# Performance work log

Hardware: AMD Instinct MI355X
Metric: run time of the kernel (lower is better)

The kernel has to match this reference:

```python
import jax, jax.numpy as jnp
import numpy as np

B, N, M = 2, 8192, 8192


def setup_inputs() -> dict:
    key = jax.random.key(0)
    ks = jax.random.split(key, 6)
    return {
        "predicted_points": jax.random.normal(ks[0], (B, N, 3), dtype=jnp.float32),
        "predicted_sdfs": jax.random.normal(ks[1], (B, N, 1), dtype=jnp.float32),
        "predicted_colors": jax.random.uniform(ks[2], (B, N, 3), dtype=jnp.float32),
        "ref_points": jax.random.normal(ks[3], (B, M, 3), dtype=jnp.float32),
        "ref_sdfs": jax.random.normal(ks[4], (B, M, 1), dtype=jnp.float32),
        "ref_colors": jax.random.uniform(ks[5], (B, M, 3), dtype=jnp.float32),
    }


def reference(predicted_points, predicted_sdfs, predicted_colors,
              ref_points, ref_sdfs, ref_colors):
    # Squared pairwise distances [B, N, M]; monotonic in cdist, so argmin/min
    # match torch.cdist-based results (chamfer_distance uses squared dists).
    d2 = (jnp.sum(predicted_points ** 2, axis=-1)[:, :, None]
          + jnp.sum(ref_points ** 2, axis=-1)[:, None, :]
          - 2.0 * jnp.einsum("bnd,bmd->bnm", predicted_points, ref_points))
    d2 = jnp.maximum(d2, 0.0)

    # Faithful to original: argmin over dim=1 -> nearest PREDICTED point index
    # for each ref point, shape [B, M]; then gathers into ref_sdfs/ref_colors.
    closest = jnp.argmin(d2, axis=1)  # [B, M], values in [0, N)

    gathered_sdfs = jnp.take_along_axis(ref_sdfs, closest[..., None], axis=1)  # [B, M, 1]
    sdf_l1 = jnp.mean(jnp.abs(gathered_sdfs - predicted_sdfs))

    gathered_colors = jnp.take_along_axis(ref_colors, closest[..., None], axis=1)  # [B, M, 3]
    color_l1 = jnp.mean(jnp.abs(gathered_colors - predicted_colors))

    # pytorch3d chamfer_distance: mean over points of squared min dists in both
    # directions, summed, then mean over batch.
    cham_xy = jnp.mean(jnp.min(d2, axis=2), axis=1)  # pred -> ref, [B]
    cham_yx = jnp.mean(jnp.min(d2, axis=1), axis=1)  # ref -> pred, [B]
    chamfer = jnp.mean(cham_xy + cham_yx)

    # [sdf_l1_loss, color_l1_loss, chamfer_distance_loss]
    return jnp.stack([sdf_l1, color_l1, chamfer])
```

## Files before the change

kernel.cpp:

```cpp
#include <hip/hip_runtime.h>
#include <cstdint>
#include <cstddef>

#define B_ 2
#define N_ 8192
#define M_ 8192
#define COLSPLIT 8
#define CCHUNK (N_ / COLSPLIT)
#define NTILES (CCHUNK / 32)
#define ROWBLKS (M_ / 128)
#define RBLOCKS ((B_ * M_) / 256)

typedef __attribute__((ext_vector_type(8))) short short8;
typedef __attribute__((ext_vector_type(16))) float f32x16;

union FragU { uint4 u; short8 s; };

__device__ __forceinline__ unsigned bf16r(float f) {
    unsigned u = __float_as_uint(f);
    return ((u + 0x7FFFu + ((u >> 16) & 1u)) >> 16) & 0xFFFFu;
}
#define BF_ONE 0x3F80u

__device__ __forceinline__ unsigned umin_(unsigned a, unsigned b) { return a < b ? a : b; }
__device__ __forceinline__ unsigned long long ullmin_(unsigned long long a, unsigned long long b) { return a < b ? a : b; }

__global__ __launch_bounds__(256) void k_init(uint4* __restrict__ p)
{
    const int i = blockIdx.x * 256 + threadIdx.x;
    uint4 v = {0xFFFFFFFFu, 0xFFFFFFFFu, 0xFFFFFFFFu, 0xFFFFFFFFu};
    p[i] = v;
}

__global__ __launch_bounds__(256, 4) void k_pairs(
    const float* __restrict__ pred_pts,
    const float* __restrict__ ref_pts,
    unsigned long long* __restrict__ rowpart,
    unsigned int* __restrict__ colminU,
    float* __restrict__ out)
{
    __shared__ uint4 ldsB[CCHUNK + 1];
    __shared__ unsigned int ldsCol[CCHUNK];

    const int t    = threadIdx.x;
    const int wave = t >> 6;
    const int lane = t & 63;
    const int l31  = lane & 31;
    const int half = lane >> 5;
    const int rowblk  = blockIdx.x;
    const int cs      = blockIdx.y;
    const int colbase = cs * CCHUNK;
    const int b       = blockIdx.z;

    if (rowblk == 0 && cs == 0 && b == 0 && t == 0) {
        out[0] = 0.f; out[1] = 0.f; out[2] = 0.f;
    }

    for (int i = t; i < CCHUNK; i += 256) {
        const float* p = pred_pts + ((size_t)b * N_ + colbase + i) * 3;
        float x = p[0], y = p[1], z = p[2];
        float nrm = x * x + y * y + z * z;
        unsigned nh = bf16r(nrm);
        unsigned nl = bf16r(nrm - __uint_as_float(nh << 16));
        uint4 v;
        v.x = bf16r(-2.f * x) | (bf16r(-2.f * y) << 16);
        v.y = bf16r(-2.f * z) | (BF_ONE << 16);
        v.z = BF_ONE | (nh << 16);
        v.w = nl;
        ldsB[i] = v;
        ldsCol[i] = 0xFFFFFFFFu;
    }
    if (t == 0) { uint4 z4 = {0, 0, 0, 0}; ldsB[CCHUNK] = z4; }

    FragU af; af.u.x = af.u.y = af.u.z = af.u.w = 0;
    const int rowbase = rowblk * 128 + wave * 32;
    if (half == 0) {
        const float* r = ref_pts + ((size_t)b * M_ + rowbase + l31) * 3;
        float x = r[0], y = r[1], z = r[2];
        float nrm = x * x + y * y + z * z;
        unsigned nh = bf16r(nrm);
        unsigned nl = bf16r(nrm - __uint_as_float(nh << 16));
        af.u.x = bf16r(x) | (bf16r(y) << 16);
        af.u.y = bf16r(z) | (nh << 16);
        af.u.z = nl | (BF_ONE << 16);
        af.u.w = BF_ONE;
    }
    __syncthreads();

    f32x16 zero16 = {};
    unsigned rowbest[16];
    #pragma unroll
    for (int i = 0; i < 16; ++i) rowbest[i] = 0xFFFFFFFFu;

    const int bslot = (half == 0) ? l31 : CCHUNK;
    const int bstep = (half == 0) ? 32 : 0;

    #pragma unroll 2
    for (int tile = 0; tile < NTILES; tile += 2) {
        FragU b0; b0.u = ldsB[bslot + tile * bstep];
        FragU b1; b1.u = ldsB[bslot + (tile + 1) * bstep];
        f32x16 acc0 = __builtin_amdgcn_mfma_f32_32x32x16_bf16(af.s, b0.s, zero16, 0, 0, 0);
        f32x16 acc1 = __builtin_amdgcn_mfma_f32_32x32x16_bf16(af.s, b1.s, zero16, 0, 0, 0);

        const unsigned lcol0 = (unsigned)(tile * 32 + l31);
        const unsigned lcol1 = lcol0 + 32;
        #pragma unroll
        for (int i = 0; i < 16; ++i) {
            unsigned pk0 = (__float_as_uint(acc0[i]) & 0xFFFFF800u) | lcol0;
            unsigned pk1 = (__float_as_uint(acc1[i]) & 0xFFFFF800u) | lcol1;
            rowbest[i] = umin_(rowbest[i], umin_(pk0, pk1));
        }
        float c0 = fminf(fminf(fminf(fminf(acc0[0], acc0[1]), fminf(acc0[2], acc0[3])),
                               fminf(fminf(acc0[4], acc0[5]), fminf(acc0[6], acc0[7]))),
                         fminf(fminf(fminf(acc0[8], acc0[9]), fminf(acc0[10], acc0[11])),
                               fminf(fminf(acc0[12], acc0[13]), fminf(acc0[14], acc0[15]))));
        float c1 = fminf(fminf(fminf(fminf(acc1[0], acc1[1]), fminf(acc1[2], acc1[3])),
                               fminf(fminf(acc1[4], acc1[5]), fminf(acc1[6], acc1[7]))),
                         fminf(fminf(fminf(acc1[8], acc1[9]), fminf(acc1[10], acc1[11])),
                               fminf(fminf(acc1[12], acc1[13]), fminf(acc1[14], acc1[15]))));
        atomicMin(&ldsCol[lcol0], __float_as_uint(c0));
        atomicMin(&ldsCol[lcol1], __float_as_uint(c1));
    }

    unsigned long long* rdst = rowpart + (size_t)(b * COLSPLIT + cs) * M_;
    #pragma unroll
    for (int i = 0; i < 16; ++i) {
        unsigned pk = rowbest[i];
        #pragma unroll
        for (int off = 1; off < 32; off <<= 1) {
            unsigned o = __shfl_xor(pk, off);
            pk = o < pk ? o : pk;
        }
        if (l31 == 0) {
            int row = rowbase + (i & 3) + 8 * (i >> 2) + 4 * half;
            rdst[row] = ((unsigned long long)(pk & 0xFFFFF800u) << 32)
                        | (unsigned)(colbase + (pk & 0x7FFu));
        }
    }

    __syncthreads();
    for (int i = t; i < CCHUNK; i += 256)
        atomicMin(&colminU[(size_t)b * N_ + colbase + i], ldsCol[i]);
}

__global__ __launch_bounds__(256) void k_reduce(
    const unsigned long long* __restrict__ rowpart,
    const unsigned int* __restrict__ colminU,
    const float* __restrict__ pred_sdfs,
    const float* __restrict__ pred_cols,
    const float* __restrict__ ref_sdfs,
    const float* __restrict__ ref_cols,
    float* __restrict__ out)
{
    __shared__ float wsum[4][3];
    const int i = blockIdx.x * 256 + threadIdx.x;
    const int b = i >> 13;
    const int m = i & (M_ - 1);

    unsigned long long pk = 0xFFFFFFFFFFFFFFFFull;
    #pragma unroll
    for (int s = 0; s < COLSPLIT; ++s)
        pk = ullmin_(pk, rowpart[(size_t)(b * COLSPLIT + s) * M_ + m]);

    unsigned cm = colminU[i];

    float chyx = fmaxf(__uint_as_float((unsigned)(pk >> 32)), 0.f);
    int arg = (int)(unsigned)(pk & 0xFFFFFFFFull);
    float chxy = fmaxf(__uint_as_float(cm), 0.f);

    float sdf = fabsf(ref_sdfs[(size_t)b * M_ + arg] - pred_sdfs[i]);
    const float* rc = ref_cols + ((size_t)b * M_ + arg) * 3;
    const float* pc = pred_cols + (size_t)i * 3;
    float col = fabsf(rc[0] - pc[0]) + fabsf(rc[1] - pc[1]) + fabsf(rc[2] - pc[2]);

    float cham = chyx * (1.f / (B_ * M_)) + chxy * (1.f / (B_ * N_));
    sdf *= 1.f / (B_ * M_);
    col *= 1.f / (B_ * M_ * 3);

    #pragma unroll
    for (int off = 32; off > 0; off >>= 1) {
        sdf  += __shfl_down(sdf, off);
        col  += __shfl_down(col, off);
        cham += __shfl_down(cham, off);
    }
    const int wave = threadIdx.x >> 6;
    if ((threadIdx.x & 63) == 0) {
        wsum[wave][0] = sdf; wsum[wave][1] = col; wsum[wave][2] = cham;
    }
    __syncthreads();
    if (threadIdx.x == 0) {
        atomicAdd(&out[0], wsum[0][0] + wsum[1][0] + wsum[2][0] + wsum[3][0]);
        atomicAdd(&out[1], wsum[0][1] + wsum[1][1] + wsum[2][1] + wsum[3][1]);
        atomicAdd(&out[2], wsum[0][2] + wsum[1][2] + wsum[2][2] + wsum[3][2]);
    }
}

extern "C" void kernel_launch(void* const* d_in, const int* in_sizes, int n_in,
                              void* d_out, int out_size, void* d_ws, size_t ws_size,
                              hipStream_t stream) {
    const float* pred_pts  = (const float*)d_in[0];
    const float* pred_sdfs = (const float*)d_in[1];
    const float* pred_cols = (const float*)d_in[2];
    const float* ref_pts   = (const float*)d_in[3];
    const float* ref_sdfs  = (const float*)d_in[4];
    const float* ref_cols  = (const float*)d_in[5];
    float* out = (float*)d_out;

    char* ws = (char*)d_ws;
    unsigned long long* rowpart = (unsigned long long*)ws;
    unsigned int* colminU = (unsigned int*)(ws + (size_t)B_ * COLSPLIT * M_ * 8);

    k_init<<<16, 256, 0, stream>>>((uint4*)colminU);

    dim3 g1(ROWBLKS, COLSPLIT, B_);
    k_pairs<<<g1, 256, 0, stream>>>(pred_pts, ref_pts, rowpart, colminU, out);

    k_reduce<<<RBLOCKS, 256, 0, stream>>>(
        rowpart, colminU, pred_sdfs, pred_cols, ref_sdfs, ref_cols, out);
}
```

Baseline: 90.61 us.

## Precompute bf16 point fragments once and double the column split

```diff
diff --git a/kernel.cpp b/kernel.cpp
--- a/kernel.cpp
+++ b/kernel.cpp
@@ -5,7 +5,7 @@
 #define B_ 2
 #define N_ 8192
 #define M_ 8192
-#define COLSPLIT 8
+#define COLSPLIT 16
 #define CCHUNK (N_ / COLSPLIT)
 #define NTILES (CCHUNK / 32)
 #define ROWBLKS (M_ / 128)
@@ -25,19 +25,55 @@
 __device__ __forceinline__ unsigned umin_(unsigned a, unsigned b) { return a < b ? a : b; }
 __device__ __forceinline__ unsigned long long ullmin_(unsigned long long a, unsigned long long b) { return a < b ? a : b; }
 
-__global__ __launch_bounds__(256) void k_init(uint4* __restrict__ p)
+__global__ __launch_bounds__(256) void k_init(
+    const float* __restrict__ pred_pts,
+    const float* __restrict__ ref_pts,
+    uint4* __restrict__ predB,
+    uint4* __restrict__ refA,
+    uint4* __restrict__ colminU4,
+    float* __restrict__ out)
 {
     const int i = blockIdx.x * 256 + threadIdx.x;
-    uint4 v = {0xFFFFFFFFu, 0xFFFFFFFFu, 0xFFFFFFFFu, 0xFFFFFFFFu};
-    p[i] = v;
+
+    if (i == 0) { out[0] = 0.f; out[1] = 0.f; out[2] = 0.f; }
+    if (i < (B_ * N_) / 4) {
+        uint4 v = {0xFFFFFFFFu, 0xFFFFFFFFu, 0xFFFFFFFFu, 0xFFFFFFFFu};
+        colminU4[i] = v;
+    }
+
+    {
+        const float* p = pred_pts + (size_t)i * 3;
+        float x = p[0], y = p[1], z = p[2];
+        float nrm = x * x + y * y + z * z;
+        unsigned nh = bf16r(nrm);
+        unsigned nl = bf16r(nrm - __uint_as_float(nh << 16));
+        uint4 v;
+        v.x = bf16r(-2.f * x) | (bf16r(-2.f * y) << 16);
+        v.y = bf16r(-2.f * z) | (BF_ONE << 16);
+        v.z = BF_ONE | (nh << 16);
+        v.w = nl;
+        predB[i] = v;
+    }
+    {
+        const float* r = ref_pts + (size_t)i * 3;
+        float x = r[0], y = r[1], z = r[2];
+        float nrm = x * x + y * y + z * z;
+        unsigned nh = bf16r(nrm);
+        unsigned nl = bf16r(nrm - __uint_as_float(nh << 16));
+        uint4 v;
+        v.x = bf16r(x) | (bf16r(y) << 16);
+        v.y = bf16r(z) | (nh << 16);
+        v.z = nl | (BF_ONE << 16);
+        v.w = BF_ONE;
+        refA[i] = v;
+    }
 }
 
 __global__ __launch_bounds__(256, 4) void k_pairs(
-    const float* __restrict__ pred_pts,
-    const float* __restrict__ ref_pts,
+    const uint4* __restrict__ predB,
+    const uint4* __restrict__ refA,
     unsigned long long* __restrict__ rowpart,
-    unsigned int* __restrict__ colminU,
-    float* __restrict__ out)
+    unsigned int* __restrict__ colminU)
 {
     __shared__ uint4 ldsB[CCHUNK + 1];
     __shared__ unsigned int ldsCol[CCHUNK];
@@ -52,39 +88,17 @@
     const int colbase = cs * CCHUNK;
     const int b       = blockIdx.z;
 
-    if (rowblk == 0 && cs == 0 && b == 0 && t == 0) {
-        out[0] = 0.f; out[1] = 0.f; out[2] = 0.f;
-    }
-
+    #pragma unroll
     for (int i = t; i < CCHUNK; i += 256) {
-        const float* p = pred_pts + ((size_t)b * N_ + colbase + i) * 3;
-        float x = p[0], y = p[1], z = p[2];
-        float nrm = x * x + y * y + z * z;
-        unsigned nh = bf16r(nrm);
-        unsigned nl = bf16r(nrm - __uint_as_float(nh << 16));
-        uint4 v;
-        v.x = bf16r(-2.f * x) | (bf16r(-2.f * y) << 16);
-        v.y = bf16r(-2.f * z) | (BF_ONE << 16);
-        v.z = BF_ONE | (nh << 16);
-        v.w = nl;
-        ldsB[i] = v;
+        ldsB[i] = predB[(size_t)b * N_ + colbase + i];
         ldsCol[i] = 0xFFFFFFFFu;
     }
     if (t == 0) { uint4 z4 = {0, 0, 0, 0}; ldsB[CCHUNK] = z4; }
 
-    FragU af; af.u.x = af.u.y = af.u.z = af.u.w = 0;
     const int rowbase = rowblk * 128 + wave * 32;
-    if (half == 0) {
-        const float* r = ref_pts + ((size_t)b * M_ + rowbase + l31) * 3;
-        float x = r[0], y = r[1], z = r[2];
-        float nrm = x * x + y * y + z * z;
-        unsigned nh = bf16r(nrm);
-        unsigned nl = bf16r(nrm - __uint_as_float(nh << 16));
-        af.u.x = bf16r(x) | (bf16r(y) << 16);
-        af.u.y = bf16r(z) | (nh << 16);
-        af.u.z = nl | (BF_ONE << 16);
-        af.u.w = BF_ONE;
-    }
+    FragU af;
+    if (half == 0) af.u = refA[(size_t)b * M_ + rowbase + l31];
+    else           { af.u.x = af.u.y = af.u.z = af.u.w = 0; }
     __syncthreads();
 
     f32x16 zero16 = {};
@@ -139,6 +153,7 @@
     }
 
     __syncthreads();
+    #pragma unroll
     for (int i = t; i < CCHUNK; i += 256)
         atomicMin(&colminU[(size_t)b * N_ + colbase + i], ldsCol[i]);
 }
@@ -209,11 +224,14 @@
     char* ws = (char*)d_ws;
     unsigned long long* rowpart = (unsigned long long*)ws;
     unsigned int* colminU = (unsigned int*)(ws + (size_t)B_ * COLSPLIT * M_ * 8);
-
-    k_init<<<16, 256, 0, stream>>>((uint4*)colminU);
+    uint4* predB = (uint4*)(ws + (size_t)B_ * COLSPLIT * M_ * 8 + (size_t)B_ * N_ * 4);
+    uint4* refA  = predB + (size_t)B_ * N_;
+
+    k_init<<<(B_ * N_) / 256, 256, 0, stream>>>(
+        pred_pts, ref_pts, predB, refA, (uint4*)colminU, out);
 
     dim3 g1(ROWBLKS, COLSPLIT, B_);
-    k_pairs<<<g1, 256, 0, stream>>>(pred_pts, ref_pts, rowpart, colminU, out);
+    k_pairs<<<g1, 256, 0, stream>>>(predB, refA, rowpart, colminU);
 
     k_reduce<<<RBLOCKS, 256, 0, stream>>>(
         rowpart, colminU, pred_sdfs, pred_cols, ref_sdfs, ref_cols, out);
```

Result: slower. 93.05 us (+2.7%).
